# Kernel tuning notes

Measured on AMD Instinct MI355X. Metric: run time of the kernel, lower is better.

Reference implementation:

```python
import jax, jax.numpy as jnp
import numpy as np

B, Q, C = 1024, 300, 80   # batch, queries, classes
K = 300                   # num_top_queries


def setup_inputs() -> dict:
    key = jax.random.key(0)
    k1, k2, k3 = jax.random.split(key, 3)
    pred_logits = jax.random.normal(k1, (B, Q, C), dtype=jnp.float32)
    # cxcywh boxes normalized to [0,1]
    pred_boxes = jax.random.uniform(k2, (B, Q, 4), dtype=jnp.float32)
    # original image sizes (w, h) in pixels
    orig_target_sizes = jax.random.uniform(k3, (B, 2), dtype=jnp.float32) * 1333.0 + 1.0
    return {"pred_logits": pred_logits, "pred_boxes": pred_boxes,
            "orig_target_sizes": orig_target_sizes}


def reference(pred_logits, pred_boxes, orig_target_sizes):
    # box_convert cxcywh -> xyxy
    cx, cy, w, h = jnp.split(pred_boxes, 4, axis=-1)
    xyxy = jnp.concatenate([cx - 0.5 * w, cy - 0.5 * h,
                            cx + 0.5 * w, cy + 0.5 * h], axis=-1)  # [B,Q,4]
    # scale by (w,h,w,h) per image
    scale = jnp.tile(orig_target_sizes, (1, 2))[:, None, :]          # [B,1,4]
    bbox_pred = xyxy * scale                                         # [B,Q,4]

    # focal-loss branch: sigmoid + flattened topk
    scores_flat = jax.nn.sigmoid(pred_logits).reshape(B, Q * C)      # [B,Q*C]
    top_scores, index = jax.lax.top_k(scores_flat, K)                # [B,K]
    labels = index % C                                               # class id
    qidx = index // C                                                # query id
    boxes = jnp.take_along_axis(bbox_pred, qidx[..., None], axis=1)  # [B,K,4]
    return labels, boxes, top_scores
```

## Files before the change

### kernel.cpp

```cpp
#include <hip/hip_runtime.h>
#include <stdint.h>

#define NBATCH 1024
#define NQ 300
#define NC 80
#define QC 24000
#define NF4 6000
#define TOPK 300
#define RSEL 384u
#define NT 512
#define NB1 2048
#define SH1 21
#define SH2 13
#define SELCAP 2048
#define FINCAP 768
#define TAIL 368
#define THRESH 2.0f
#define NBH 2048
#define SBASE 0x3F600000u

__device__ __forceinline__ uint32_t xform(uint32_t u) {
    return u ^ (uint32_t)(((int32_t)u >> 31) | 0x80000000);
}

__device__ __forceinline__ uint32_t sbucket(uint32_t sbits) {
    int32_t d = (int32_t)(sbits - SBASE);
    d = d < 0 ? 0 : d;
    uint32_t bkt = ((uint32_t)d) >> 10;
    return bkt > (NBH - 1) ? (NBH - 1) : bkt;
}

template<int NB, bool ZERO>
__device__ __forceinline__ void pick(uint32_t* __restrict__ hist,
                                     uint32_t* __restrict__ part,
                                     uint32_t* __restrict__ gsufx,
                                     uint32_t* __restrict__ misc,
                                     int tid, uint32_t rem,
                                     uint32_t* bucket_out, uint32_t* rem_out) {
    constexpr int G = (NB >= NT) ? (NB / NT) : 1;
    const int base = tid * G;
    uint32_t h[G];
    uint32_t s = 0;
    if (base < NB) {
#pragma unroll
        for (int u = 0; u < G; ++u) { h[u] = hist[base + u]; s += h[u]; }
        if (ZERO) {
#pragma unroll
            for (int u = 0; u < G; ++u) hist[base + u] = 0;
        }
    } else {
#pragma unroll
        for (int u = 0; u < G; ++u) h[u] = 0;
    }
    part[tid] = s;
    __syncthreads();

    if (tid < 64) {
        uint32_t gs = 0;
#pragma unroll
        for (int u = 0; u < 8; ++u) gs += part[(tid << 3) + u];
        uint32_t S = gs;
#pragma unroll
        for (int off = 1; off < 64; off <<= 1) {
            uint32_t v = __shfl_down(S, off, 64);
            if (tid + off < 64) S += v;
        }
        gsufx[tid] = S;
        if (tid == 0) gsufx[64] = 0;
    }
    __syncthreads();

    const int g8 = tid >> 3;
    uint32_t A = gsufx[g8 + 1];
    for (int t2 = tid + 1; t2 < ((g8 + 1) << 3); ++t2) A += part[t2];
    if (base < NB && A < rem && A + s >= rem) {
        uint32_t acc = 0, bsel = (uint32_t)base, r = 1;
#pragma unroll
        for (int u = G - 1; u >= 0; --u) {
            if (A + acc + h[u] >= rem) { bsel = (uint32_t)(base + u); r = rem - A - acc; break; }
            acc += h[u];
        }
        misc[0] = bsel;
        misc[1] = r;
    }
    __syncthreads();
    *bucket_out = misc[0];
    *rem_out    = misc[1];
}

__global__ void __launch_bounds__(NT, 6)
rtdetr_post_kernel(const float* __restrict__ logits, const float* __restrict__ pboxes,
                   const float* __restrict__ sizes, float* __restrict__ out) {
    __shared__ __align__(16) uint32_t hist[NBH + 1];
    __shared__ uint64_t sel[SELCAP];
    __shared__ uint64_t sel2[FINCAP];
    __shared__ uint32_t part[NT];
    __shared__ uint32_t gsufx[65];
    __shared__ uint32_t misc[4];

    const int tid = threadIdx.x;
    const int b   = blockIdx.x;
    const float4* lg4 = reinterpret_cast<const float4*>(logits + (size_t)b * QC);

    for (int i = tid; i <= NBH; i += NT) hist[i] = 0;
    if (tid == 0) { misc[2] = 0; misc[3] = 0; }
    __syncthreads();

#pragma unroll
    for (int k = 0; k < 12; ++k) {
        if (k < 11 || tid < TAIL) {
            float4 v = lg4[tid + (k << 9)];
            const uint32_t i4 = (uint32_t)(tid + (k << 9));
            float f[4] = { v.x, v.y, v.z, v.w };
#pragma unroll
            for (int c = 0; c < 4; ++c) {
                if (f[c] >= THRESH) {
                    uint32_t key = xform(__float_as_uint(f[c]));
                    uint32_t pos = atomicAdd(&misc[2], 1u);
                    uint32_t idx = 4u * i4 + (uint32_t)c;
                    if (pos < SELCAP)
                        sel[pos] = ((uint64_t)key << 32) | (uint64_t)(0xFFFFFFFFu - idx);
                }
            }
        }
    }
    __syncthreads();

    const uint32_t cnt = misc[2];
    uint32_t n2;

    if (cnt >= RSEL && cnt <= FINCAP) {
        for (uint32_t i = tid; i < cnt; i += NT) {
            uint64_t e = sel[i];
            uint32_t k = (uint32_t)(e >> 32);
            uint32_t bits = (k & 0x80000000u) ? (k & 0x7FFFFFFFu) : ~k;
            float x  = __uint_as_float(bits);
            float sc = 1.0f / (1.0f + expf(-x));
            sel2[i] = ((uint64_t)__float_as_uint(sc) << 32) | (uint64_t)(uint32_t)e;
        }
        n2 = cnt;
    } else {
        for (int i4 = tid; i4 < NF4; i4 += NT) {
            float4 v = lg4[i4];
            atomicAdd(&hist[xform(__float_as_uint(v.x)) >> SH1], 1u);
            atomicAdd(&hist[xform(__float_as_uint(v.y)) >> SH1], 1u);
            atomicAdd(&hist[xform(__float_as_uint(v.z)) >> SH1], 1u);
            atomicAdd(&hist[xform(__float_as_uint(v.w)) >> SH1], 1u);
        }
        __syncthreads();
        uint32_t b1, r1;
        pick<NB1, true>(hist, part, gsufx, misc, tid, RSEL, &b1, &r1);
        if (tid == 0) misc[2] = 0;
        __syncthreads();
        for (int i4 = tid; i4 < NF4; i4 += NT) {
            float4 v = lg4[i4];
            uint32_t kk[4] = { xform(__float_as_uint(v.x)), xform(__float_as_uint(v.y)),
                               xform(__float_as_uint(v.z)), xform(__float_as_uint(v.w)) };
#pragma unroll
            for (int c = 0; c < 4; ++c) {
                uint32_t k = kk[c];
                uint32_t bk = k >> SH1;
                if (bk >= b1) {
                    uint32_t pos = atomicAdd(&misc[2], 1u);
                    uint32_t idx = 4u * (uint32_t)i4 + (uint32_t)c;
                    if (pos < SELCAP)
                        sel[pos] = ((uint64_t)k << 32) | (uint64_t)(0xFFFFFFFFu - idx);
                    if (bk == b1) atomicAdd(&hist[(k >> SH2) & 0xFFu], 1u);
                }
            }
        }
        __syncthreads();
        uint32_t t2, r2;
        pick<256, false>(hist, part, gsufx, misc, tid, r1, &t2, &r2);
        (void)r2;
        const uint32_t T2 = (b1 << SH1) | (t2 << SH2);
        uint32_t c2 = misc[2];
        uint32_t nn = c2 > SELCAP ? SELCAP : c2;
        for (uint32_t i = tid; i < nn; i += NT) {
            uint64_t e = sel[i];
            uint32_t k = (uint32_t)(e >> 32);
            if (k >= T2) {
                uint32_t bits = (k & 0x80000000u) ? (k & 0x7FFFFFFFu) : ~k;
                float x  = __uint_as_float(bits);
                float sc = 1.0f / (1.0f + expf(-x));
                uint32_t pos = atomicAdd(&misc[3], 1u);
                if (pos < FINCAP)
                    sel2[pos] = ((uint64_t)__float_as_uint(sc) << 32) | (uint64_t)(uint32_t)e;
            }
        }
        __syncthreads();
        uint32_t m3 = misc[3];
        n2 = m3 > FINCAP ? FINCAP : m3;
        for (int i = tid; i < 256; i += NT) hist[i] = 0;
    }
    __syncthreads();

    for (uint32_t i = tid; i < n2; i += NT)
        atomicAdd(&hist[sbucket((uint32_t)(sel2[i] >> 32))], 1u);
    __syncthreads();

    {
        const int base = tid * (NBH / NT);
        uint32_t h0 = hist[base], h1 = hist[base + 1], h2 = hist[base + 2], h3 = hist[base + 3];
        part[tid] = h0 + h1 + h2 + h3;
        __syncthreads();
        if (tid < 64) {
            uint32_t gs = 0;
#pragma unroll
            for (int u = 0; u < 8; ++u) gs += part[(tid << 3) + u];
            uint32_t S = gs;
#pragma unroll
            for (int off = 1; off < 64; off <<= 1) {
                uint32_t v = __shfl_down(S, off, 64);
                if (tid + off < 64) S += v;
            }
            gsufx[tid] = S;
            if (tid == 0) gsufx[64] = 0;
        }
        __syncthreads();
        const int g8 = tid >> 3;
        uint32_t A = gsufx[g8 + 1];
        for (int t2 = tid + 1; t2 < ((g8 + 1) << 3); ++t2) A += part[t2];
        hist[base + 3] = A;
        hist[base + 2] = A + h3;
        hist[base + 1] = A + h3 + h2;
        hist[base + 0] = A + h3 + h2 + h1;
    }
    __syncthreads();

    for (uint32_t i = tid; i < n2; i += NT) {
        uint64_t k = sel2[i];
        uint32_t slot = atomicAdd(&hist[sbucket((uint32_t)(k >> 32))], 1u);
        sel[slot] = k;
    }
    __syncthreads();

    for (uint32_t i = tid; i < n2; i += NT) {
        uint64_t my = sel2[i];
        uint32_t bkt = sbucket((uint32_t)(my >> 32));
        uint32_t seg0 = hist[bkt + 1];
        uint32_t seg1 = hist[bkt];
        uint32_t rank = seg0;
        for (uint32_t j = seg0; j < seg1; ++j)
            rank += (sel[j] > my) ? 1u : 0u;
        if (rank < TOPK) {
            uint32_t idx = 0xFFFFFFFFu - (uint32_t)(my & 0xFFFFFFFFull);
            uint32_t lab = idx % NC;
            uint32_t q   = idx / NC;
            float4 bx = reinterpret_cast<const float4*>(pboxes)[(size_t)b * NQ + q];
            float sw = sizes[2 * b + 0];
            float sh = sizes[2 * b + 1];
            float hw = 0.5f * bx.z, hh = 0.5f * bx.w;
            float4 o;
            o.x = (bx.x - hw) * sw;
            o.y = (bx.y - hh) * sh;
            o.z = (bx.x + hw) * sw;
            o.w = (bx.y + hh) * sh;
            out[(size_t)b * TOPK + rank] = (float)lab;
            reinterpret_cast<float4*>(out + (size_t)NBATCH * TOPK)[(size_t)b * TOPK + rank] = o;
            out[(size_t)NBATCH * TOPK * 5 + (size_t)b * TOPK + rank] =
                __uint_as_float((uint32_t)(my >> 32));
        }
    }
}

extern "C" void kernel_launch(void* const* d_in, const int* in_sizes, int n_in,
                              void* d_out, int out_size, void* d_ws, size_t ws_size,
                              hipStream_t stream) {
    const float* logits = (const float*)d_in[0];
    const float* pboxes = (const float*)d_in[1];
    const float* sizes  = (const float*)d_in[2];
    float* out = (float*)d_out;

    hipLaunchKernelGGL(rtdetr_post_kernel, dim3(NBATCH), dim3(NT), 0, stream,
                       logits, pboxes, sizes, out);
}
```

Measured before the change: 25.25 us.

## Stream logits into LDS with async global_load_lds in a three-deep pipeline

The first thresholding pass now issues `global_load_lds` copies of 16 bytes per lane into a per-wave LDS staging ring, three slots deep. Each iteration reads its slot and refills it with the chunk three iterations ahead. This is meant to keep more loads in flight and hide global latency on a memory-bound scan. SELCAP is halved so the new staging buffer fits in LDS. Total LDS still grows, which may reduce resident blocks per CU, and correctness depends on the compiler inserting proper waits before the LDS reads.

Result: slower. 32.50 us (+28.7%).

```diff
diff --git a/kernel.cpp b/kernel.cpp
--- a/kernel.cpp
+++ b/kernel.cpp
@@ -9,10 +9,12 @@
 #define TOPK 300
 #define RSEL 384u
 #define NT 512
+#define NWAVE 8
+#define DEPTH 3
 #define NB1 2048
 #define SH1 21
 #define SH2 13
-#define SELCAP 2048
+#define SELCAP 1024
 #define FINCAP 768
 #define TAIL 368
 #define THRESH 2.0f
@@ -28,6 +30,13 @@
     d = d < 0 ? 0 : d;
     uint32_t bkt = ((uint32_t)d) >> 10;
     return bkt > (NBH - 1) ? (NBH - 1) : bkt;
+}
+
+__device__ __forceinline__ void async_load16(const float4* gsrc, float4* ldst) {
+    __builtin_amdgcn_global_load_lds(
+        (const __attribute__((address_space(1))) void*)gsrc,
+        (__attribute__((address_space(3))) void*)ldst,
+        16, 0, 0);
 }
 
 template<int NB, bool ZERO>
@@ -91,15 +100,18 @@
 __global__ void __launch_bounds__(NT, 6)
 rtdetr_post_kernel(const float* __restrict__ logits, const float* __restrict__ pboxes,
                    const float* __restrict__ sizes, float* __restrict__ out) {
-    __shared__ __align__(16) uint32_t hist[NBH + 1];
-    __shared__ uint64_t sel[SELCAP];
-    __shared__ uint64_t sel2[FINCAP];
+    __shared__ float4   stage[NWAVE][DEPTH][64];
+    __shared__ uint64_t cand[SELCAP];
+    __shared__ uint64_t srt[FINCAP];
+    __shared__ uint32_t hist[NBH + 1];
     __shared__ uint32_t part[NT];
     __shared__ uint32_t gsufx[65];
     __shared__ uint32_t misc[4];
 
-    const int tid = threadIdx.x;
-    const int b   = blockIdx.x;
+    const int tid  = threadIdx.x;
+    const int lane = tid & 63;
+    const int wave = tid >> 6;
+    const int b    = blockIdx.x;
     const float4* lg4 = reinterpret_cast<const float4*>(logits + (size_t)b * QC);
 
     for (int i = tid; i <= NBH; i += NT) hist[i] = 0;
@@ -107,21 +119,30 @@
     __syncthreads();
 
 #pragma unroll
+    for (int j = 0; j < DEPTH; ++j)
+        async_load16(lg4 + (tid + (j << 9)), &stage[wave][j][0]);
+
+#pragma unroll
     for (int k = 0; k < 12; ++k) {
+        float4 v = stage[wave][k % DEPTH][lane];
         if (k < 11 || tid < TAIL) {
-            float4 v = lg4[tid + (k << 9)];
-            const uint32_t i4 = (uint32_t)(tid + (k << 9));
+            const int i4 = tid + (k << 9);
             float f[4] = { v.x, v.y, v.z, v.w };
 #pragma unroll
             for (int c = 0; c < 4; ++c) {
                 if (f[c] >= THRESH) {
                     uint32_t key = xform(__float_as_uint(f[c]));
                     uint32_t pos = atomicAdd(&misc[2], 1u);
-                    uint32_t idx = 4u * i4 + (uint32_t)c;
+                    uint32_t idx = 4u * (uint32_t)i4 + (uint32_t)c;
                     if (pos < SELCAP)
-                        sel[pos] = ((uint64_t)key << 32) | (uint64_t)(0xFFFFFFFFu - idx);
+                        cand[pos] = ((uint64_t)key << 32) | (uint64_t)(0xFFFFFFFFu - idx);
                 }
             }
+        }
+        if (k + DEPTH < 12) {
+            int i4n = tid + ((k + DEPTH) << 9);
+            if (i4n > NF4 - 1) i4n = NF4 - 1;
+            async_load16(lg4 + i4n, &stage[wave][k % DEPTH][0]);
         }
     }
     __syncthreads();
@@ -131,15 +152,17 @@
 
     if (cnt >= RSEL && cnt <= FINCAP) {
         for (uint32_t i = tid; i < cnt; i += NT) {
-            uint64_t e = sel[i];
+            uint64_t e = cand[i];
             uint32_t k = (uint32_t)(e >> 32);
             uint32_t bits = (k & 0x80000000u) ? (k & 0x7FFFFFFFu) : ~k;
             float x  = __uint_as_float(bits);
             float sc = 1.0f / (1.0f + expf(-x));
-            sel2[i] = ((uint64_t)__float_as_uint(sc) << 32) | (uint64_t)(uint32_t)e;
+            srt[i] = ((uint64_t)__float_as_uint(sc) << 32) | (uint64_t)(uint32_t)e;
         }
         n2 = cnt;
     } else {
+        if (tid == 0) misc[2] = 0;
+        __syncthreads();
         for (int i4 = tid; i4 < NF4; i4 += NT) {
             float4 v = lg4[i4];
             atomicAdd(&hist[xform(__float_as_uint(v.x)) >> SH1], 1u);
@@ -150,8 +173,6 @@
         __syncthreads();
         uint32_t b1, r1;
         pick<NB1, true>(hist, part, gsufx, misc, tid, RSEL, &b1, &r1);
-        if (tid == 0) misc[2] = 0;
-        __syncthreads();
         for (int i4 = tid; i4 < NF4; i4 += NT) {
             float4 v = lg4[i4];
             uint32_t kk[4] = { xform(__float_as_uint(v.x)), xform(__float_as_uint(v.y)),
@@ -164,7 +185,7 @@
                     uint32_t pos = atomicAdd(&misc[2], 1u);
                     uint32_t idx = 4u * (uint32_t)i4 + (uint32_t)c;
                     if (pos < SELCAP)
-                        sel[pos] = ((uint64_t)k << 32) | (uint64_t)(0xFFFFFFFFu - idx);
+                        cand[pos] = ((uint64_t)k << 32) | (uint64_t)(0xFFFFFFFFu - idx);
                     if (bk == b1) atomicAdd(&hist[(k >> SH2) & 0xFFu], 1u);
                 }
             }
@@ -177,7 +198,7 @@
         uint32_t c2 = misc[2];
         uint32_t nn = c2 > SELCAP ? SELCAP : c2;
         for (uint32_t i = tid; i < nn; i += NT) {
-            uint64_t e = sel[i];
+            uint64_t e = cand[i];
             uint32_t k = (uint32_t)(e >> 32);
             if (k >= T2) {
                 uint32_t bits = (k & 0x80000000u) ? (k & 0x7FFFFFFFu) : ~k;
@@ -185,7 +206,7 @@
                 float sc = 1.0f / (1.0f + expf(-x));
                 uint32_t pos = atomicAdd(&misc[3], 1u);
                 if (pos < FINCAP)
-                    sel2[pos] = ((uint64_t)__float_as_uint(sc) << 32) | (uint64_t)(uint32_t)e;
+                    srt[pos] = ((uint64_t)__float_as_uint(sc) << 32) | (uint64_t)(uint32_t)e;
             }
         }
         __syncthreads();
@@ -196,7 +217,7 @@
     __syncthreads();
 
     for (uint32_t i = tid; i < n2; i += NT)
-        atomicAdd(&hist[sbucket((uint32_t)(sel2[i] >> 32))], 1u);
+        atomicAdd(&hist[sbucket((uint32_t)(srt[i] >> 32))], 1u);
     __syncthreads();
 
     {
@@ -229,20 +250,20 @@
     __syncthreads();
 
     for (uint32_t i = tid; i < n2; i += NT) {
-        uint64_t k = sel2[i];
+        uint64_t k = srt[i];
         uint32_t slot = atomicAdd(&hist[sbucket((uint32_t)(k >> 32))], 1u);
-        sel[slot] = k;
+        cand[slot] = k;
     }
     __syncthreads();
 
     for (uint32_t i = tid; i < n2; i += NT) {
-        uint64_t my = sel2[i];
+        uint64_t my = srt[i];
         uint32_t bkt = sbucket((uint32_t)(my >> 32));
         uint32_t seg0 = hist[bkt + 1];
         uint32_t seg1 = hist[bkt];
         uint32_t rank = seg0;
         for (uint32_t j = seg0; j < seg1; ++j)
-            rank += (sel[j] > my) ? 1u : 0u;
+            rank += (cand[j] > my) ? 1u : 0u;
         if (rank < TOPK) {
             uint32_t idx = 0xFFFFFFFFu - (uint32_t)(my & 0xFFFFFFFFull);
             uint32_t lab = idx % NC;
```
